# Kernel optimization log

Hardware: AMD Instinct MI355X
Metric: run time of the kernel (lower is better)

Reference implementation:

```python
import jax, jax.numpy as jnp
import numpy as np

EMBED_DIM = 1024
NUM_HEADS = 16
HEAD_DIM = EMBED_DIM // NUM_HEADS
SCALE = HEAD_DIM ** -0.5


def setup_inputs() -> dict:
    key = jax.random.key(0)
    k_x, k_qkv, k_proj = jax.random.split(key, 3)
    x = jax.random.normal(k_x, (2, 2048, EMBED_DIM), dtype=jnp.float32)
    # nn.Linear weights: [out_features, in_features]
    w_qkv = jax.random.normal(k_qkv, (3 * EMBED_DIM, EMBED_DIM), dtype=jnp.float32) * (EMBED_DIM ** -0.5)
    w_proj = jax.random.normal(k_proj, (EMBED_DIM, EMBED_DIM), dtype=jnp.float32) * (EMBED_DIM ** -0.5)
    return {"x": x, "w_qkv": w_qkv, "w_proj": w_proj}


def reference(x, w_qkv, w_proj):
    B, N, C = x.shape
    # fused QKV projection: [B,N,3C]
    qkv = jnp.einsum('bnc,oc->bno', x, w_qkv)
    qkv = qkv.reshape(B, N, 3, NUM_HEADS, HEAD_DIM)
    q, k, v = jnp.moveaxis(qkv, 2, 0)  # each [B, N, H, D]
    q = q.transpose(0, 2, 1, 3)  # [B, H, N, D]
    k = k.transpose(0, 2, 1, 3)
    v = v.transpose(0, 2, 1, 3)
    # scaled dot-product attention (eval mode: dropout_p=0, non-causal)
    scores = jnp.einsum('bhqd,bhkd->bhqk', q, k) * SCALE
    attn = jax.nn.softmax(scores, axis=-1)
    out = jnp.einsum('bhqk,bhkd->bhqd', attn, v)  # [B, H, N, D]
    out = out.transpose(0, 2, 1, 3).reshape(B, N, C)
    return jnp.einsum('bnc,oc->bno', out, w_proj)
```

## Files before the change

### kernel.cpp

```cpp
#include <hip/hip_runtime.h>
#include <hip/hip_bf16.h>

typedef __bf16 bf16;
typedef __bf16 bf16x8 __attribute__((ext_vector_type(8)));
typedef __bf16 bf16x4 __attribute__((ext_vector_type(4)));
typedef _Float16 f16;
typedef _Float16 f16x4 __attribute__((ext_vector_type(4)));
typedef float f32x4 __attribute__((ext_vector_type(4)));

#define MFMA16(a, b, c)    __builtin_amdgcn_mfma_f32_16x16x32_bf16(a, b, c, 0, 0, 0)
#define MFMA16F16(a, b, c) __builtin_amdgcn_mfma_f32_16x16x16f16(a, b, c, 0, 0, 0)

__device__ __forceinline__ void gll(const void* g, void* l) {
    __builtin_amdgcn_global_load_lds(
        (const __attribute__((address_space(1))) unsigned int*)g,
        (__attribute__((address_space(3))) unsigned int*)l, 16, 0, 0);
}

__global__ void cvt_all(const float* __restrict__ x, const float* __restrict__ wq,
                        const float* __restrict__ wp, bf16* __restrict__ xb,
                        bf16* __restrict__ wqb, bf16* __restrict__ wpb) {
    int i = blockIdx.x * 256 + threadIdx.x;
    const float4* s; bf16* d; int j;
    if (i < 1048576)                { s = (const float4*)x;  d = xb;  j = i; }
    else if (i < 1048576 + 786432)  { s = (const float4*)wq; d = wqb; j = i - 1048576; }
    else                            { s = (const float4*)wp; d = wpb; j = i - 1835008; }
    float4 f = s[j];
    bf16x4 o; o[0] = (bf16)f.x; o[1] = (bf16)f.y; o[2] = (bf16)f.z; o[3] = (bf16)f.w;
    ((bf16x4*)d)[j] = o;
}

#define QSCALE 0.18033688f

__global__ __launch_bounds__(256, 3) void gemm_qkv(
    const bf16* __restrict__ A, const bf16* __restrict__ Bm,
    bf16* __restrict__ qo, bf16* __restrict__ ko, f16* __restrict__ vo)
{
    __shared__ bf16 As[2][128 * 32];
    __shared__ bf16 Bs[2][128 * 32];
    const int tid = threadIdx.x;
    const int wave = tid >> 6, lane = tid & 63;
    const int lrow = lane & 15, quad = lane >> 4;
    const int wm = (wave >> 1) * 64, wn = (wave & 1) * 64;
    const int srow = tid >> 2;
    const int scol = ((tid & 3) ^ (srow & 3)) * 8;
    const int fsw = (quad ^ (lrow & 3)) * 8;

    const bf16* Ap = A + (long)(blockIdx.x * 128 + srow) * 1024 + scol;
    const bf16* Bp = Bm + (long)(blockIdx.y * 128 + srow) * 1024 + scol;

    f32x4 acc[4][4] = {};
    const int gm0 = blockIdx.x * 128 + wm;
    const int go0 = blockIdx.y * 128 + wn;

    gll(Ap, &As[0][tid * 8]);  gll(Ap + 64 * 1024, &As[0][2048 + tid * 8]);
    gll(Bp, &Bs[0][tid * 8]);  gll(Bp + 64 * 1024, &Bs[0][2048 + tid * 8]);

    if (blockIdx.y < 16) {
        for (int i = 0; i < 32; i++) {
            const int cur = i & 1;
            __syncthreads();
            if (i < 31) {
                const int k0 = (i + 1) * 32;
                gll(Ap + k0, &As[cur ^ 1][tid * 8]);
                gll(Ap + 64 * 1024 + k0, &As[cur ^ 1][2048 + tid * 8]);
                gll(Bp + k0, &Bs[cur ^ 1][tid * 8]);
                gll(Bp + 64 * 1024 + k0, &Bs[cur ^ 1][2048 + tid * 8]);
            }
            bf16x8 af[4], bfr[4];
#pragma unroll
            for (int ii = 0; ii < 4; ii++) af[ii] = *(const bf16x8*)&As[cur][(wm + ii * 16 + lrow) * 32 + fsw];
#pragma unroll
            for (int j = 0; j < 4; j++) bfr[j] = *(const bf16x8*)&Bs[cur][(wn + j * 16 + lrow) * 32 + fsw];
#pragma unroll
            for (int ii = 0; ii < 4; ii++)
#pragma unroll
                for (int j = 0; j < 4; j++)
                    acc[ii][j] = MFMA16(bfr[j], af[ii], acc[ii][j]);
        }
        const bool isQ = blockIdx.y < 8;
        bf16* dst = isQ ? qo : ko;
        const float sc = isQ ? QSCALE : 1.0f;
#pragma unroll
        for (int i = 0; i < 4; i++) {
            int gm = gm0 + i * 16 + lrow;
            int b = gm >> 11, n = gm & 2047;
#pragma unroll
            for (int j = 0; j < 4; j++) {
                int ob = go0 + j * 16 + quad * 4;
                int rem = ob & 1023;
                int h = rem >> 6, d0 = rem & 63;
                bf16x4 pk;
#pragma unroll
                for (int r = 0; r < 4; r++) pk[r] = (bf16)(acc[i][j][r] * sc);
                *(bf16x4*)&dst[((long)(b * 16 + h) * 2048 + n) * 64 + d0] = pk;
            }
        }
    } else {
        for (int i = 0; i < 32; i++) {
            const int cur = i & 1;
            __syncthreads();
            if (i < 31) {
                const int k0 = (i + 1) * 32;
                gll(Ap + k0, &As[cur ^ 1][tid * 8]);
                gll(Ap + 64 * 1024 + k0, &As[cur ^ 1][2048 + tid * 8]);
                gll(Bp + k0, &Bs[cur ^ 1][tid * 8]);
                gll(Bp + 64 * 1024 + k0, &Bs[cur ^ 1][2048 + tid * 8]);
            }
            bf16x8 af[4], bfr[4];
#pragma unroll
            for (int ii = 0; ii < 4; ii++) af[ii] = *(const bf16x8*)&As[cur][(wm + ii * 16 + lrow) * 32 + fsw];
#pragma unroll
            for (int j = 0; j < 4; j++) bfr[j] = *(const bf16x8*)&Bs[cur][(wn + j * 16 + lrow) * 32 + fsw];
#pragma unroll
            for (int ii = 0; ii < 4; ii++)
#pragma unroll
                for (int j = 0; j < 4; j++)
                    acc[ii][j] = MFMA16(af[ii], bfr[j], acc[ii][j]);
        }
#pragma unroll
        for (int i = 0; i < 4; i++) {
            int gmb = gm0 + i * 16 + quad * 4;
            int b = gmb >> 11, nb = gmb & 2047;
#pragma unroll
            for (int j = 0; j < 4; j++) {
                int o = go0 + j * 16 + lrow;
                int rem = o & 1023;
                int h = rem >> 6, d = rem & 63;
                f16x4 pk;
#pragma unroll
                for (int r = 0; r < 4; r++) pk[r] = (f16)acc[i][j][r];
                *(f16x4*)&vo[(((long)(b * 16 + h)) * 64 + d) * 2048 + nb] = pk;
            }
        }
    }
}

__global__ __launch_bounds__(256, 2) void attn_kernel(
    const bf16* __restrict__ q, const bf16* __restrict__ k,
    const f16* __restrict__ vt, bf16* __restrict__ o)
{
    __shared__ bf16  Ks[2][64 * 64];
    __shared__ f16   Vs[2][64 * 64];
    __shared__ float Pt[2][64 * 68];
    __shared__ float lsumL[2][64];

    const int tid = threadIdx.x, wave = tid >> 6, lane = tid & 63;
    const int lrow = lane & 15, quad = lane >> 4;
    const int qh = wave & 1, kh = wave >> 1;
    const int bh = blockIdx.x & 31, qt = blockIdx.x >> 5;
    const bf16* Qp = q + ((long)bh * 2048 + qt * 128 + qh * 64) * 64;
    const bf16* Kp = k + (long)bh * 2048 * 64;
    const f16*  Vp = vt + (long)bh * 64 * 2048;

    const int sr = tid >> 3;
    const int scc = ((tid & 7) ^ (sr & 7)) * 8;

    bf16x8 qf[4][2];
#pragma unroll
    for (int t = 0; t < 4; t++)
#pragma unroll
        for (int ks = 0; ks < 2; ks++)
            qf[t][ks] = *(const bf16x8*)&Qp[(t * 16 + lrow) * 64 + ks * 32 + quad * 8];

#pragma unroll
    for (int p = 0; p < 2; p++) {
        gll(Kp + (sr + 32 * p) * 64 + scc,         &Ks[0][p * 2048 + tid * 8]);
        gll(Vp + (long)(sr + 32 * p) * 2048 + scc, &Vs[0][p * 2048 + tid * 8]);
    }

    float lsum[4] = {0.f, 0.f, 0.f, 0.f};
    f32x4 oacc[4][4] = {};

    for (int kv = 0; kv < 32; kv++) {
        const int cur = kv & 1;
        __syncthreads();
        if (kv < 31) {
            const bf16* Kn = Kp + (kv + 1) * 4096;
            const f16*  Vn = Vp + (kv + 1) * 64;
#pragma unroll
            for (int p = 0; p < 2; p++) {
                gll(Kn + (sr + 32 * p) * 64 + scc,         &Ks[cur ^ 1][p * 2048 + tid * 8]);
                gll(Vn + (long)(sr + 32 * p) * 2048 + scc, &Vs[cur ^ 1][p * 2048 + tid * 8]);
            }
        }

        f32x4 sacc[4][2];
#pragma unroll
        for (int t = 0; t < 4; t++)
#pragma unroll
            for (int n = 0; n < 2; n++) sacc[t][n] = f32x4{-8.f, -8.f, -8.f, -8.f};
#pragma unroll
        for (int ks = 0; ks < 2; ks++) {
            bf16x8 kf[2];
#pragma unroll
            for (int n = 0; n < 2; n++)
                kf[n] = *(const bf16x8*)&Ks[cur][(kh * 32 + n * 16 + lrow) * 64 +
                                                 (((ks * 4 + quad) ^ (lrow & 7)) * 8)];
#pragma unroll
            for (int t = 0; t < 4; t++)
#pragma unroll
                for (int n = 0; n < 2; n++)
                    sacc[t][n] = MFMA16(kf[n], qf[t][ks], sacc[t][n]);
        }

        f16x4 pa[4][2];
#pragma unroll
        for (int t = 0; t < 4; t++)
#pragma unroll
            for (int n = 0; n < 2; n++)
#pragma unroll
                for (int r = 0; r < 4; r++) {
                    float p = __builtin_exp2f(sacc[t][n][r]);
                    lsum[t] += p;
                    pa[t][n][r] = (f16)p;
                }

#pragma unroll
        for (int jd = 0; jd < 4; jd++) {
            f16x4 vf[2];
#pragma unroll
            for (int n = 0; n < 2; n++) {
                int cs = kh * 4 + n * 2 + (quad >> 1);
                vf[n] = *(const f16x4*)&Vs[cur][(jd * 16 + lrow) * 64 +
                                               ((cs ^ (lrow & 7)) * 8) + (quad & 1) * 4];
            }
#pragma unroll
            for (int t = 0; t < 4; t++)
#pragma unroll
                for (int n = 0; n < 2; n++)
                    oacc[t][jd] = MFMA16F16(pa[t][n], vf[n], oacc[t][jd]);
        }
    }

#pragma unroll
    for (int t = 0; t < 4; t++) {
        lsum[t] += __shfl_xor(lsum[t], 16, 64);
        lsum[t] += __shfl_xor(lsum[t], 32, 64);
    }

    float* Pr = &Pt[qh][0];
    if (kh == 1) {
#pragma unroll
        for (int t = 0; t < 4; t++)
#pragma unroll
            for (int jd = 0; jd < 4; jd++)
                *(f32x4*)&Pr[lane * 68 + (t * 4 + jd) * 4] = oacc[t][jd];
        if (quad == 0)
#pragma unroll
            for (int t = 0; t < 4; t++) lsumL[qh][t * 16 + lrow] = lsum[t];
    }
    __syncthreads();
    if (kh == 0) {
#pragma unroll
        for (int t = 0; t < 4; t++)
#pragma unroll
            for (int jd = 0; jd < 4; jd++)
                oacc[t][jd] += *(const f32x4*)&Pr[lane * 68 + (t * 4 + jd) * 4];
#pragma unroll
        for (int t = 0; t < 4; t++) lsum[t] += lsumL[qh][t * 16 + lrow];

        bf16* Tw = (bf16*)Pr;
        const int b = bh >> 4, h = bh & 15;
#pragma unroll
        for (int t = 0; t < 4; t++) {
            float linv = 1.0f / lsum[t];
#pragma unroll
            for (int r = 0; r < 4; r++) {
                float lr = __shfl(linv, quad * 4 + r, 64);
#pragma unroll
                for (int jd = 0; jd < 4; jd++)
                    Tw[(t * 16 + quad * 4 + r) * 72 + jd * 16 + lrow] = (bf16)(oacc[t][jd][r] * lr);
            }
        }
        const int rr = lane >> 3, cc = (lane & 7) * 8;
#pragma unroll
        for (int p = 0; p < 8; p++) {
            bf16x8 val = *(const bf16x8*)&Tw[(rr + p * 8) * 72 + cc];
            int n = qt * 128 + qh * 64 + rr + p * 8;
            *(bf16x8*)&o[((long)(b * 2048 + n)) * 1024 + h * 64 + cc] = val;
        }
    }
}

__global__ __launch_bounds__(256, 2) void gemm_proj(
    const bf16* __restrict__ A, const bf16* __restrict__ Bm, float* __restrict__ out)
{
    __shared__ bf16 As[2][128 * 32];
    __shared__ bf16 Bs[2][64 * 32];
    const int tid = threadIdx.x;
    const int wave = tid >> 6, lane = tid & 63;
    const int lrow = lane & 15, quad = lane >> 4;
    const int wm = (wave >> 1) * 64, wn = (wave & 1) * 32;
    const int srow = tid >> 2;
    const int scol = ((tid & 3) ^ (srow & 3)) * 8;
    const int fsw = (quad ^ (lrow & 3)) * 8;

    const bf16* Ap = A + (long)(blockIdx.x * 128 + srow) * 1024 + scol;
    const bf16* Bp = Bm + (long)(blockIdx.y * 64 + srow) * 1024 + scol;

    f32x4 acc[4][2] = {};

    gll(Ap, &As[0][tid * 8]);  gll(Ap + 64 * 1024, &As[0][2048 + tid * 8]);
    gll(Bp, &Bs[0][tid * 8]);

    for (int i = 0; i < 32; i++) {
        const int cur = i & 1;
        __syncthreads();
        if (i < 31) {
            const int k0 = (i + 1) * 32;
            gll(Ap + k0, &As[cur ^ 1][tid * 8]);
            gll(Ap + 64 * 1024 + k0, &As[cur ^ 1][2048 + tid * 8]);
            gll(Bp + k0, &Bs[cur ^ 1][tid * 8]);
        }
        bf16x8 af[4], bfr[2];
#pragma unroll
        for (int ii = 0; ii < 4; ii++) af[ii] = *(const bf16x8*)&As[cur][(wm + ii * 16 + lrow) * 32 + fsw];
#pragma unroll
        for (int j = 0; j < 2; j++) bfr[j] = *(const bf16x8*)&Bs[cur][(wn + j * 16 + lrow) * 32 + fsw];
#pragma unroll
        for (int ii = 0; ii < 4; ii++)
#pragma unroll
            for (int j = 0; j < 2; j++)
                acc[ii][j] = MFMA16(bfr[j], af[ii], acc[ii][j]);
    }

    const int gm0 = blockIdx.x * 128 + wm;
    const int go0 = blockIdx.y * 64 + wn;
#pragma unroll
    for (int i = 0; i < 4; i++) {
        int gm = gm0 + i * 16 + lrow;
#pragma unroll
        for (int j = 0; j < 2; j++) {
            int ob = go0 + j * 16 + quad * 4;
            *(f32x4*)&out[(long)gm * 1024 + ob] = acc[i][j];
        }
    }
}

extern "C" void kernel_launch(void* const* d_in, const int* in_sizes, int n_in,
                              void* d_out, int out_size, void* d_ws, size_t ws_size,
                              hipStream_t stream) {
    const float* x      = (const float*)d_in[0];
    const float* w_qkv  = (const float*)d_in[1];
    const float* w_proj = (const float*)d_in[2];
    float* out = (float*)d_out;

    bf16* ws = (bf16*)d_ws;
    bf16* xb     = ws;
    bf16* wqkvb  = xb + 4096 * 1024;
    bf16* wprojb = wqkvb + 3072 * 1024;
    bf16* qb     = wprojb + 1024 * 1024;
    bf16* kb     = qb + 2 * 16 * 2048 * 64;
    f16*  vb     = (f16*)(kb + 2 * 16 * 2048 * 64);
    bf16* ob     = (bf16*)(vb + 2 * 16 * 2048 * 64);

    cvt_all<<<8192, 256, 0, stream>>>(x, w_qkv, w_proj, xb, wqkvb, wprojb);
    gemm_qkv<<<dim3(32, 24), 256, 0, stream>>>(xb, wqkvb, qb, kb, vb);
    attn_kernel<<<512, 256, 0, stream>>>(qb, kb, vb, ob);
    gemm_proj<<<dim3(32, 16), 256, 0, stream>>>(ob, wprojb, out);
}
```

Baseline: 193.2 us.

## Stream V fragments directly from global and deepen K prefetch to four-stage ring

The attention kernel stops staging V tiles through LDS and instead loads each lane's f16x4 V fragments straight from global memory into registers at the top of each KV iteration. K moves to a 4-slot LDS ring prefetched two tiles ahead, with a manual vmcnt wait and a raw s_barrier replacing __syncthreads. MFMA sections are wrapped in s_setprio, and the LDS is unioned into one char buffer reused for the epilogue reduction. This aims to cut LDS traffic and barrier stalls, but the uncoalesced 8-byte global V loads and hand-counted vmcnt waits risk higher memory latency and fragile ordering.

```diff
diff --git a/kernel.cpp b/kernel.cpp
--- a/kernel.cpp
+++ b/kernel.cpp
@@ -140,10 +140,8 @@
     const bf16* __restrict__ q, const bf16* __restrict__ k,
     const f16* __restrict__ vt, bf16* __restrict__ o)
 {
-    __shared__ bf16  Ks[2][64 * 64];
-    __shared__ f16   Vs[2][64 * 64];
-    __shared__ float Pt[2][64 * 68];
-    __shared__ float lsumL[2][64];
+    __shared__ __align__(16) char smem[35328];
+    bf16* KsB = (bf16*)smem;
 
     const int tid = threadIdx.x, wave = tid >> 6, lane = tid & 63;
     const int lrow = lane & 15, quad = lane >> 4;
@@ -162,47 +160,59 @@
 #pragma unroll
         for (int ks = 0; ks < 2; ks++)
             qf[t][ks] = *(const bf16x8*)&Qp[(t * 16 + lrow) * 64 + ks * 32 + quad * 8];
-
-#pragma unroll
-    for (int p = 0; p < 2; p++) {
-        gll(Kp + (sr + 32 * p) * 64 + scc,         &Ks[0][p * 2048 + tid * 8]);
-        gll(Vp + (long)(sr + 32 * p) * 2048 + scc, &Vs[0][p * 2048 + tid * 8]);
-    }
-
+    asm volatile("s_waitcnt vmcnt(0)" ::: "memory");
+
+#pragma unroll
+    for (int b = 0; b < 2; b++) {
+        gll(Kp + b * 4096 + sr * 64 + scc,        KsB + b * 4096 + tid * 8);
+        gll(Kp + b * 4096 + (sr + 32) * 64 + scc, KsB + b * 4096 + 2048 + tid * 8);
+    }
+
+    f32x4 oacc[4][4] = {};
     float lsum[4] = {0.f, 0.f, 0.f, 0.f};
-    f32x4 oacc[4][4] = {};
 
     for (int kv = 0; kv < 32; kv++) {
-        const int cur = kv & 1;
-        __syncthreads();
-        if (kv < 31) {
-            const bf16* Kn = Kp + (kv + 1) * 4096;
-            const f16*  Vn = Vp + (kv + 1) * 64;
-#pragma unroll
-            for (int p = 0; p < 2; p++) {
-                gll(Kn + (sr + 32 * p) * 64 + scc,         &Ks[cur ^ 1][p * 2048 + tid * 8]);
-                gll(Vn + (long)(sr + 32 * p) * 2048 + scc, &Vs[cur ^ 1][p * 2048 + tid * 8]);
-            }
-        }
-
+        asm volatile("s_waitcnt vmcnt(2)" ::: "memory");
+        __builtin_amdgcn_s_barrier();
+        asm volatile("" ::: "memory");
+
+        f16x4 vfr[2][4];
+#pragma unroll
+        for (int n = 0; n < 2; n++)
+#pragma unroll
+            for (int jd = 0; jd < 4; jd++)
+                vfr[n][jd] = *(const f16x4*)&Vp[(long)(jd * 16 + lrow) * 2048 +
+                                                kv * 64 + kh * 32 + n * 16 + quad * 4];
+
+        if (kv < 30) {
+            bf16* kd = KsB + ((kv + 2) & 3) * 4096;
+            gll(Kp + (kv + 2) * 4096 + sr * 64 + scc,        kd + tid * 8);
+            gll(Kp + (kv + 2) * 4096 + (sr + 32) * 64 + scc, kd + 2048 + tid * 8);
+        }
+
+        const bf16* Kc = KsB + (kv & 3) * 4096;
+
+        bf16x8 kf[2][2];
+#pragma unroll
+        for (int ks = 0; ks < 2; ks++)
+#pragma unroll
+            for (int n = 0; n < 2; n++)
+                kf[ks][n] = *(const bf16x8*)&Kc[(kh * 32 + n * 16 + lrow) * 64 +
+                                                (((ks * 4 + quad) ^ (lrow & 7)) * 8)];
         f32x4 sacc[4][2];
 #pragma unroll
         for (int t = 0; t < 4; t++)
 #pragma unroll
             for (int n = 0; n < 2; n++) sacc[t][n] = f32x4{-8.f, -8.f, -8.f, -8.f};
-#pragma unroll
-        for (int ks = 0; ks < 2; ks++) {
-            bf16x8 kf[2];
-#pragma unroll
-            for (int n = 0; n < 2; n++)
-                kf[n] = *(const bf16x8*)&Ks[cur][(kh * 32 + n * 16 + lrow) * 64 +
-                                                 (((ks * 4 + quad) ^ (lrow & 7)) * 8)];
+        __builtin_amdgcn_s_setprio(1);
+#pragma unroll
+        for (int ks = 0; ks < 2; ks++)
 #pragma unroll
             for (int t = 0; t < 4; t++)
 #pragma unroll
                 for (int n = 0; n < 2; n++)
-                    sacc[t][n] = MFMA16(kf[n], qf[t][ks], sacc[t][n]);
-        }
+                    sacc[t][n] = MFMA16(kf[ks][n], qf[t][ks], sacc[t][n]);
+        __builtin_amdgcn_s_setprio(0);
 
         f16x4 pa[4][2];
 #pragma unroll
@@ -216,21 +226,15 @@
                     pa[t][n][r] = (f16)p;
                 }
 
-#pragma unroll
-        for (int jd = 0; jd < 4; jd++) {
-            f16x4 vf[2];
-#pragma unroll
-            for (int n = 0; n < 2; n++) {
-                int cs = kh * 4 + n * 2 + (quad >> 1);
-                vf[n] = *(const f16x4*)&Vs[cur][(jd * 16 + lrow) * 64 +
-                                               ((cs ^ (lrow & 7)) * 8) + (quad & 1) * 4];
-            }
+        __builtin_amdgcn_s_setprio(1);
+#pragma unroll
+        for (int jd = 0; jd < 4; jd++)
 #pragma unroll
             for (int t = 0; t < 4; t++)
 #pragma unroll
                 for (int n = 0; n < 2; n++)
-                    oacc[t][jd] = MFMA16F16(pa[t][n], vf[n], oacc[t][jd]);
-        }
+                    oacc[t][jd] = MFMA16F16(pa[t][n], vfr[n][jd], oacc[t][jd]);
+        __builtin_amdgcn_s_setprio(0);
     }
 
 #pragma unroll
@@ -239,7 +243,10 @@
         lsum[t] += __shfl_xor(lsum[t], 32, 64);
     }
 
-    float* Pr = &Pt[qh][0];
+    __syncthreads();
+    float* Pt  = (float*)smem;
+    float* lsL = (float*)(smem + 34816);
+    float* Pr  = Pt + qh * (64 * 68);
     if (kh == 1) {
 #pragma unroll
         for (int t = 0; t < 4; t++)
@@ -248,7 +255,7 @@
                 *(f32x4*)&Pr[lane * 68 + (t * 4 + jd) * 4] = oacc[t][jd];
         if (quad == 0)
 #pragma unroll
-            for (int t = 0; t < 4; t++) lsumL[qh][t * 16 + lrow] = lsum[t];
+            for (int t = 0; t < 4; t++) lsL[qh * 64 + t * 16 + lrow] = lsum[t];
     }
     __syncthreads();
     if (kh == 0) {
@@ -258,7 +265,7 @@
             for (int jd = 0; jd < 4; jd++)
                 oacc[t][jd] += *(const f32x4*)&Pr[lane * 68 + (t * 4 + jd) * 4];
 #pragma unroll
-        for (int t = 0; t < 4; t++) lsum[t] += lsumL[qh][t * 16 + lrow];
+        for (int t = 0; t < 4; t++) lsum[t] += lsL[qh * 64 + t * 16 + lrow];
 
         bf16* Tw = (bf16*)Pr;
         const int b = bh >> 4, h = bh & 15;
```

Result: slower. 205.0 us (+6.1%).
